# Kernel optimization log

Measured on AMD Instinct MI355X. Metric: run time of the kernel, lower is better.

## Reference

```python
import jax, jax.numpy as jnp
import numpy as np

ZERO_POINT = 128  # asymmetric int8 zero point
LORA_ALPHA = 16.0
LORA_R = 64
LORA_SCALING = LORA_ALPHA / LORA_R


def setup_inputs() -> dict:
    key = jax.random.key(0)
    k_x, k_w, k_s, k_a, k_b, k_bias = jax.random.split(key, 6)
    B, S, D_in, D_out, R = 64, 1, 8192, 8192, LORA_R
    x = jax.random.normal(k_x, (B, S, D_in), dtype=jnp.float32)
    W_q = jax.random.randint(k_w, (D_out, D_in), 0, 256, dtype=jnp.int32)
    scale = jax.random.uniform(k_s, (D_out,), dtype=jnp.float32) * 0.02
    lora_A = jax.random.normal(k_a, (R, D_in), dtype=jnp.float32) * 0.02
    lora_B = jax.random.normal(k_b, (D_out, R), dtype=jnp.float32) * 0.02
    bias = jax.random.normal(k_bias, (D_out,), dtype=jnp.float32)
    return {"x": x, "W_q": W_q, "scale": scale, "lora_A": lora_A,
            "lora_B": lora_B, "bias": bias}


def reference(x, W_q, scale, lora_A, lora_B, bias):
    # Dequantize frozen base weight: per-output-channel asymmetric int8.
    # W_deq[o, i] = (W_q[o, i] - zero_point) * scale[o]
    W_deq = (W_q.astype(jnp.float32) - ZERO_POINT) * scale[:, None]  # [O, I]
    # Base quantized linear: y = x @ W_deq^T + bias
    base = jnp.einsum('bsi,oi->bso', x, W_deq) + bias  # [B, S, O]
    # LoRA low-rank path: (alpha/r) * (x @ A^T) @ B^T  (dropout = 0.0)
    lora_mid = jnp.einsum('bsi,ri->bsr', x, lora_A)        # [B, S, r]
    lora_out = jnp.einsum('bsr,or->bso', lora_mid, lora_B)  # [B, S, O]
    return base + LORA_SCALING * lora_out
```

## Files before the change

### kernel.cpp

```cpp
#include <hip/hip_runtime.h>
#include <stdint.h>

#define B_ 64
#define K_ 8192
#define O_ 8192
#define R_ 64
#define NT 16
#define BK 128
#define NSTEP (K_ / BK)

typedef __attribute__((ext_vector_type(8))) short s16x8;
typedef __attribute__((ext_vector_type(4))) float f32x4;

__device__ __forceinline__ uint32_t rne_pack(float a, float b) {
  uint32_t ua = __float_as_uint(a), ub = __float_as_uint(b);
  ua += 0x7fffu + ((ua >> 16) & 1u);
  ub += 0x7fffu + ((ub >> 16) & 1u);
  return (ua >> 16) | (ub & 0xffff0000u);
}

__device__ __forceinline__ uint32_t wpack(int w0, int w1) {
  float f0 = (float)(w0 - 128);
  float f1 = (float)(w1 - 128);
  return (__float_as_uint(f0) >> 16) | (__float_as_uint(f1) & 0xffff0000u);
}

__global__ __launch_bounds__(256) void k_prep(
    const float* __restrict__ x, const float* __restrict__ lora_A,
    uint16_t* __restrict__ xbg, float* __restrict__ mid) {
  const int t = threadIdx.x;
  const int blk = blockIdx.x;

  {
    const size_t base = (size_t)blk * 2048 + (size_t)t * 8;
    float4 v0 = *(const float4*)(x + base);
    float4 v1 = *(const float4*)(x + base + 4);
    uint4 p;
    p.x = rne_pack(v0.x, v0.y);
    p.y = rne_pack(v0.z, v0.w);
    p.z = rne_pack(v1.x, v1.y);
    p.w = rne_pack(v1.z, v1.w);
    *(uint4*)(xbg + base) = p;
  }

  if (blk >= 64) return;

  __shared__ float xs[64][133];
  __shared__ float as_[64][133];
  const int kr0 = blk * BK;
  const int row = t >> 2, seg = t & 3;
#pragma unroll
  for (int j = 0; j < 8; ++j) {
    const int c = seg * 32 + j * 4;
    float4 vx = *(const float4*)(x + (size_t)row * K_ + kr0 + c);
    float4 va = *(const float4*)(lora_A + (size_t)row * K_ + kr0 + c);
    xs[row][c] = vx.x; xs[row][c + 1] = vx.y; xs[row][c + 2] = vx.z; xs[row][c + 3] = vx.w;
    as_[row][c] = va.x; as_[row][c + 1] = va.y; as_[row][c + 2] = va.z; as_[row][c + 3] = va.w;
  }
  __syncthreads();

  const int bg = t >> 4, rg = t & 15;
  const int b0 = bg * 4, r0 = rg * 4;
  float acc[4][4];
#pragma unroll
  for (int i = 0; i < 4; ++i)
#pragma unroll
    for (int j = 0; j < 4; ++j) acc[i][j] = 0.f;

  for (int k = 0; k < BK; ++k) {
    float xv[4], av[4];
#pragma unroll
    for (int i = 0; i < 4; ++i) xv[i] = xs[b0 + i][k];
#pragma unroll
    for (int j = 0; j < 4; ++j) av[j] = as_[r0 + j][k];
#pragma unroll
    for (int i = 0; i < 4; ++i)
#pragma unroll
      for (int j = 0; j < 4; ++j) acc[i][j] += xv[i] * av[j];
  }

#pragma unroll
  for (int i = 0; i < 4; ++i)
#pragma unroll
    for (int j = 0; j < 4; ++j)
      atomicAdd(&mid[(b0 + i) * R_ + (r0 + j)], acc[i][j]);
}

__global__ __launch_bounds__(256, 2) void k_main(
    const int* __restrict__ Wq, const float* __restrict__ scale,
    const float* __restrict__ lora_B, const float* __restrict__ bias,
    const uint16_t* __restrict__ xbg, const float* __restrict__ mid,
    float* __restrict__ out) {
  __shared__ uint16_t xa[2][64][136];
  __shared__ uint16_t wbs[2][NT][136];
  __shared__ uint16_t midb[64][72];
  __shared__ uint16_t lob[NT][72];

  const int t = threadIdx.x;
  const int o0 = blockIdx.x * NT;
  const int wave = t >> 6;
  const int lane = t & 63;
  const int il = lane & 15;
  const int g = lane >> 4;
  const int m0 = wave * 16;

  {
    const int row = t >> 2;
    const int r0 = (t & 3) * 16;
    const float* mp = mid + row * R_ + r0;
    float4 a0 = *(const float4*)(mp);
    float4 a1 = *(const float4*)(mp + 4);
    float4 a2 = *(const float4*)(mp + 8);
    float4 a3 = *(const float4*)(mp + 12);
    uint4 p0, p1;
    p0.x = rne_pack(a0.x, a0.y); p0.y = rne_pack(a0.z, a0.w);
    p0.z = rne_pack(a1.x, a1.y); p0.w = rne_pack(a1.z, a1.w);
    p1.x = rne_pack(a2.x, a2.y); p1.y = rne_pack(a2.z, a2.w);
    p1.z = rne_pack(a3.x, a3.y); p1.w = rne_pack(a3.z, a3.w);
    *(uint4*)&midb[row][r0] = p0;
    *(uint4*)&midb[row][r0 + 8] = p1;
    if (t < 64) {
      const int row2 = t >> 2;
      const float* lp = lora_B + (size_t)(o0 + row2) * R_ + r0;
      float4 c0 = *(const float4*)(lp);
      float4 c1 = *(const float4*)(lp + 4);
      float4 c2 = *(const float4*)(lp + 8);
      float4 c3 = *(const float4*)(lp + 12);
      uint4 q0, q1;
      q0.x = rne_pack(c0.x, c0.y); q0.y = rne_pack(c0.z, c0.w);
      q0.z = rne_pack(c1.x, c1.y); q0.w = rne_pack(c1.z, c1.w);
      q1.x = rne_pack(c2.x, c2.y); q1.y = rne_pack(c2.z, c2.w);
      q1.z = rne_pack(c3.x, c3.y); q1.w = rne_pack(c3.z, c3.w);
      *(uint4*)&lob[row2][r0] = q0;
      *(uint4*)&lob[row2][r0 + 8] = q1;
    }
  }

  const int xrow = t >> 2, xseg = t & 3;
  const int wrow = t >> 4, wseg = t & 15;
  const uint16_t* xsrc = xbg + (size_t)xrow * K_;
  const int* wsrc = Wq + (size_t)(o0 + wrow) * K_;

  uint4 rx0, rx1, rx2, rx3;
  int4 rw0, rw1;
#define LOADT(TT)                                         \
  do {                                                    \
    const int kt = (TT)*BK;                               \
    rx0 = *(const uint4*)(xsrc + kt + xseg * 32);         \
    rx1 = *(const uint4*)(xsrc + kt + xseg * 32 + 8);     \
    rx2 = *(const uint4*)(xsrc + kt + xseg * 32 + 16);    \
    rx3 = *(const uint4*)(xsrc + kt + xseg * 32 + 24);    \
    rw0 = *(const int4*)(wsrc + kt + wseg * 8);           \
    rw1 = *(const int4*)(wsrc + kt + wseg * 8 + 4);       \
  } while (0)

  LOADT(0);

  const float sc = scale[o0 + il];
  const float bi = bias[o0 + il];

  __syncthreads();

  f32x4 acc2 = {0.f, 0.f, 0.f, 0.f};
#pragma unroll
  for (int kf = 0; kf < 2; ++kf) {
    s16x8 am = *(const s16x8*)&midb[m0 + il][kf * 32 + g * 8];
    s16x8 bl = *(const s16x8*)&lob[il][kf * 32 + g * 8];
    acc2 = __builtin_amdgcn_mfma_f32_16x16x32_bf16(am, bl, acc2, 0, 0, 0);
  }

  f32x4 acc = {0.f, 0.f, 0.f, 0.f};
  int cur = 0;
  for (int tt = 0; tt < NSTEP; ++tt) {
    *(uint4*)&xa[cur][xrow][xseg * 32] = rx0;
    *(uint4*)&xa[cur][xrow][xseg * 32 + 8] = rx1;
    *(uint4*)&xa[cur][xrow][xseg * 32 + 16] = rx2;
    *(uint4*)&xa[cur][xrow][xseg * 32 + 24] = rx3;
    uint4 wv;
    wv.x = wpack(rw0.x, rw0.y);
    wv.y = wpack(rw0.z, rw0.w);
    wv.z = wpack(rw1.x, rw1.y);
    wv.w = wpack(rw1.z, rw1.w);
    *(uint4*)&wbs[cur][wrow][wseg * 8] = wv;
    __syncthreads();
    if (tt + 1 < NSTEP) LOADT(tt + 1);
#pragma unroll
    for (int kf = 0; kf < 4; ++kf) {
      s16x8 af = *(const s16x8*)&xa[cur][m0 + il][kf * 32 + g * 8];
      s16x8 bf = *(const s16x8*)&wbs[cur][il][kf * 32 + g * 8];
      acc = __builtin_amdgcn_mfma_f32_16x16x32_bf16(af, bf, acc, 0, 0, 0);
    }
    cur ^= 1;
  }
#undef LOADT

#pragma unroll
  for (int j = 0; j < 4; ++j) {
    const int b = m0 + g * 4 + j;
    out[(size_t)b * O_ + o0 + il] = sc * acc[j] + bi + 0.25f * acc2[j];
  }
}

extern "C" void kernel_launch(void* const* d_in, const int* in_sizes, int n_in,
                              void* d_out, int out_size, void* d_ws, size_t ws_size,
                              hipStream_t stream) {
  const float* x = (const float*)d_in[0];
  const int* Wq = (const int*)d_in[1];
  const float* scale = (const float*)d_in[2];
  const float* lora_A = (const float*)d_in[3];
  const float* lora_B = (const float*)d_in[4];
  const float* bias = (const float*)d_in[5];
  float* out = (float*)d_out;

  uint16_t* xbg = (uint16_t*)d_ws;
  float* mid = (float*)((char*)d_ws + (size_t)B_ * K_ * 2);

  hipMemsetAsync(mid, 0, B_ * R_ * sizeof(float), stream);
  k_prep<<<256, 256, 0, stream>>>(x, lora_A, xbg, mid);
  k_main<<<O_ / NT, 256, 0, stream>>>(Wq, scale, lora_B, bias, xbg, mid, out);
}
```

Baseline: 92.50 us.

## Prefetch two K-tiles ahead in registers and alias LoRA LDS buffers

The main GEMV loop now keeps two register sets of global loads in flight, so tiles tt+2 and tt+3 load while the current tile runs on MFMA. This deepens the pipeline to hide HBM latency on the int32 weight stream. The global access pattern changes so each lane reads interleaved 16-byte chunks, and the midb/lob LoRA buffers now alias the xa LDS buffer to cut shared memory use. The cost is more live registers (two sets of 6 vector loads) and one extra barrier, which could hurt occupancy at launch_bounds(256,2).

```diff
diff --git a/kernel.cpp b/kernel.cpp
--- a/kernel.cpp
+++ b/kernel.cpp
@@ -93,8 +93,9 @@
     float* __restrict__ out) {
   __shared__ uint16_t xa[2][64][136];
   __shared__ uint16_t wbs[2][NT][136];
-  __shared__ uint16_t midb[64][72];
-  __shared__ uint16_t lob[NT][72];
+
+  uint16_t* midb = &xa[0][0][0];
+  uint16_t* lob = midb + 64 * 72;
 
   const int t = threadIdx.x;
   const int o0 = blockIdx.x * NT;
@@ -117,8 +118,8 @@
     p0.z = rne_pack(a1.x, a1.y); p0.w = rne_pack(a1.z, a1.w);
     p1.x = rne_pack(a2.x, a2.y); p1.y = rne_pack(a2.z, a2.w);
     p1.z = rne_pack(a3.x, a3.y); p1.w = rne_pack(a3.z, a3.w);
-    *(uint4*)&midb[row][r0] = p0;
-    *(uint4*)&midb[row][r0 + 8] = p1;
+    *(uint4*)&midb[row * 72 + r0] = p0;
+    *(uint4*)&midb[row * 72 + r0 + 8] = p1;
     if (t < 64) {
       const int row2 = t >> 2;
       const float* lp = lora_B + (size_t)(o0 + row2) * R_ + r0;
@@ -131,30 +132,57 @@
       q0.z = rne_pack(c1.x, c1.y); q0.w = rne_pack(c1.z, c1.w);
       q1.x = rne_pack(c2.x, c2.y); q1.y = rne_pack(c2.z, c2.w);
       q1.z = rne_pack(c3.x, c3.y); q1.w = rne_pack(c3.z, c3.w);
-      *(uint4*)&lob[row2][r0] = q0;
-      *(uint4*)&lob[row2][r0 + 8] = q1;
+      *(uint4*)&lob[row2 * 72 + r0] = q0;
+      *(uint4*)&lob[row2 * 72 + r0 + 8] = q1;
     }
   }
 
-  const int xrow = t >> 2, xseg = t & 3;
-  const int wrow = t >> 4, wseg = t & 15;
+  const int xrow = t >> 2, xs4 = t & 3;
+  const int wrow = t >> 4, ws16 = t & 15;
   const uint16_t* xsrc = xbg + (size_t)xrow * K_;
   const int* wsrc = Wq + (size_t)(o0 + wrow) * K_;
 
-  uint4 rx0, rx1, rx2, rx3;
-  int4 rw0, rw1;
-#define LOADT(TT)                                         \
-  do {                                                    \
-    const int kt = (TT)*BK;                               \
-    rx0 = *(const uint4*)(xsrc + kt + xseg * 32);         \
-    rx1 = *(const uint4*)(xsrc + kt + xseg * 32 + 8);     \
-    rx2 = *(const uint4*)(xsrc + kt + xseg * 32 + 16);    \
-    rx3 = *(const uint4*)(xsrc + kt + xseg * 32 + 24);    \
-    rw0 = *(const int4*)(wsrc + kt + wseg * 8);           \
-    rw1 = *(const int4*)(wsrc + kt + wseg * 8 + 4);       \
+  uint4 rxa0, rxb0, rxc0, rxd0, rxa1, rxb1, rxc1, rxd1;
+  int4 rwa0, rwb0, rwa1, rwb1;
+
+#define LOADT(P, TT)                                        \
+  do {                                                      \
+    const int kt = (TT)*BK;                                 \
+    rwa##P = *(const int4*)(wsrc + kt + ws16 * 4);          \
+    rwb##P = *(const int4*)(wsrc + kt + 64 + ws16 * 4);     \
+    rxa##P = *(const uint4*)(xsrc + kt + xs4 * 8);          \
+    rxb##P = *(const uint4*)(xsrc + kt + 32 + xs4 * 8);     \
+    rxc##P = *(const uint4*)(xsrc + kt + 64 + xs4 * 8);     \
+    rxd##P = *(const uint4*)(xsrc + kt + 96 + xs4 * 8);     \
   } while (0)
 
-  LOADT(0);
+#define STORE_LDS(P)                                        \
+  do {                                                      \
+    *(uint4*)&xa[P][xrow][xs4 * 8] = rxa##P;                \
+    *(uint4*)&xa[P][xrow][32 + xs4 * 8] = rxb##P;           \
+    *(uint4*)&xa[P][xrow][64 + xs4 * 8] = rxc##P;           \
+    *(uint4*)&xa[P][xrow][96 + xs4 * 8] = rxd##P;           \
+    uint2 wv0, wv1;                                         \
+    wv0.x = wpack(rwa##P.x, rwa##P.y);                      \
+    wv0.y = wpack(rwa##P.z, rwa##P.w);                      \
+    wv1.x = wpack(rwb##P.x, rwb##P.y);                      \
+    wv1.y = wpack(rwb##P.z, rwb##P.w);                      \
+    *(uint2*)&wbs[P][wrow][ws16 * 4] = wv0;                 \
+    *(uint2*)&wbs[P][wrow][64 + ws16 * 4] = wv1;            \
+  } while (0)
+
+#define MFMA_FROM(P)                                                          \
+  do {                                                                        \
+    _Pragma("unroll")                                                         \
+    for (int kf = 0; kf < 4; ++kf) {                                          \
+      s16x8 af = *(const s16x8*)&xa[P][m0 + il][kf * 32 + g * 8];             \
+      s16x8 bf = *(const s16x8*)&wbs[P][il][kf * 32 + g * 8];                 \
+      acc = __builtin_amdgcn_mfma_f32_16x16x32_bf16(af, bf, acc, 0, 0, 0);    \
+    }                                                                         \
+  } while (0)
+
+  LOADT(0, 0);
+  LOADT(1, 1);
 
   const float sc = scale[o0 + il];
   const float bi = bias[o0 + il];
@@ -164,35 +192,27 @@
   f32x4 acc2 = {0.f, 0.f, 0.f, 0.f};
 #pragma unroll
   for (int kf = 0; kf < 2; ++kf) {
-    s16x8 am = *(const s16x8*)&midb[m0 + il][kf * 32 + g * 8];
-    s16x8 bl = *(const s16x8*)&lob[il][kf * 32 + g * 8];
+    s16x8 am = *(const s16x8*)&midb[(m0 + il) * 72 + kf * 32 + g * 8];
+    s16x8 bl = *(const s16x8*)&lob[il * 72 + kf * 32 + g * 8];
     acc2 = __builtin_amdgcn_mfma_f32_16x16x32_bf16(am, bl, acc2, 0, 0, 0);
   }
+  __syncthreads();
 
   f32x4 acc = {0.f, 0.f, 0.f, 0.f};
-  int cur = 0;
-  for (int tt = 0; tt < NSTEP; ++tt) {
-    *(uint4*)&xa[cur][xrow][xseg * 32] = rx0;
-    *(uint4*)&xa[cur][xrow][xseg * 32 + 8] = rx1;
-    *(uint4*)&xa[cur][xrow][xseg * 32 + 16] = rx2;
-    *(uint4*)&xa[cur][xrow][xseg * 32 + 24] = rx3;
-    uint4 wv;
-    wv.x = wpack(rw0.x, rw0.y);
-    wv.y = wpack(rw0.z, rw0.w);
-    wv.z = wpack(rw1.x, rw1.y);
-    wv.w = wpack(rw1.z, rw1.w);
-    *(uint4*)&wbs[cur][wrow][wseg * 8] = wv;
+  for (int tt = 0; tt < NSTEP; tt += 2) {
+    STORE_LDS(0);
     __syncthreads();
-    if (tt + 1 < NSTEP) LOADT(tt + 1);
-#pragma unroll
-    for (int kf = 0; kf < 4; ++kf) {
-      s16x8 af = *(const s16x8*)&xa[cur][m0 + il][kf * 32 + g * 8];
-      s16x8 bf = *(const s16x8*)&wbs[cur][il][kf * 32 + g * 8];
-      acc = __builtin_amdgcn_mfma_f32_16x16x32_bf16(af, bf, acc, 0, 0, 0);
-    }
-    cur ^= 1;
+    if (tt + 2 < NSTEP) LOADT(0, tt + 2);
+    MFMA_FROM(0);
+
+    STORE_LDS(1);
+    __syncthreads();
+    if (tt + 3 < NSTEP) LOADT(1, tt + 3);
+    MFMA_FROM(1);
   }
 #undef LOADT
+#undef STORE_LDS
+#undef MFMA_FROM
 
 #pragma unroll
   for (int j = 0; j < 4; ++j) {
```

New measurement: 88.75 us. 1.04x faster.

## Split-K main GEMM into per-wave register-direct tiles with separate reduction kernel

Applied to the files above, without the earlier changes.

Restructures the main GEMM so each wave owns a 16-output by 64-batch tile over one eighth of K. The wave loads W and x fragments straight from global into registers with two-stage software pipelining and drops the shared-memory staging and block barriers. Partial sums go to a workspace buffer. A new finalize kernel reduces the eight partials and applies scale, bias and the LoRA path. The goal is more parallelism and less LDS/sync overhead, at the cost of about 16 MB of extra partial-sum traffic and one more kernel launch.

```diff
diff --git a/kernel.cpp b/kernel.cpp
--- a/kernel.cpp
+++ b/kernel.cpp
@@ -5,9 +5,10 @@
 #define K_ 8192
 #define O_ 8192
 #define R_ 64
-#define NT 16
-#define BK 128
-#define NSTEP (K_ / BK)
+#define KS 8
+#define KSL (K_ / KS)
+#define BK 64
+#define NS (KSL / BK)
 
 typedef __attribute__((ext_vector_type(8))) short s16x8;
 typedef __attribute__((ext_vector_type(4))) float f32x4;
@@ -23,6 +24,17 @@
   float f0 = (float)(w0 - 128);
   float f1 = (float)(w1 - 128);
   return (__float_as_uint(f0) >> 16) | (__float_as_uint(f1) & 0xffff0000u);
+}
+
+__device__ __forceinline__ s16x8 bfrag_from(int4 a, int4 b) {
+  union { uint32_t u[4]; s16x8 v; } r;
+  r.u[0] = wpack(a.x, a.y); r.u[1] = wpack(a.z, a.w);
+  r.u[2] = wpack(b.x, b.y); r.u[3] = wpack(b.z, b.w);
+  return r.v;
+}
+
+__device__ __forceinline__ s16x8 afrag(uint4 x) {
+  union { uint4 u; s16x8 v; } r; r.u = x; return r.v;
 }
 
 __global__ __launch_bounds__(256) void k_prep(
@@ -47,7 +59,7 @@
 
   __shared__ float xs[64][133];
   __shared__ float as_[64][133];
-  const int kr0 = blk * BK;
+  const int kr0 = blk * 128;
   const int row = t >> 2, seg = t & 3;
 #pragma unroll
   for (int j = 0; j < 8; ++j) {
@@ -67,7 +79,7 @@
 #pragma unroll
     for (int j = 0; j < 4; ++j) acc[i][j] = 0.f;
 
-  for (int k = 0; k < BK; ++k) {
+  for (int k = 0; k < 128; ++k) {
     float xv[4], av[4];
 #pragma unroll
     for (int i = 0; i < 4; ++i) xv[i] = xs[b0 + i][k];
@@ -87,17 +99,95 @@
 }
 
 __global__ __launch_bounds__(256, 2) void k_main(
-    const int* __restrict__ Wq, const float* __restrict__ scale,
+    const int* __restrict__ Wq, const uint16_t* __restrict__ xbg,
+    float* __restrict__ part) {
+  const int t = threadIdx.x;
+  const int w = blockIdx.x * 4 + (t >> 6);
+  const int lane = t & 63;
+  const int il = lane & 15;
+  const int g = lane >> 4;
+  const int ks = w >> 9;
+  const int oc = w & 511;
+  const int o0 = oc * 16;
+  const int k0 = ks * KSL;
+
+  const int* wp = Wq + (size_t)(o0 + il) * K_ + k0 + g * 8;
+  const uint16_t* xp0 = xbg + (size_t)(il) * K_ + k0 + g * 8;
+  const uint16_t* xp1 = xbg + (size_t)(16 + il) * K_ + k0 + g * 8;
+  const uint16_t* xp2 = xbg + (size_t)(32 + il) * K_ + k0 + g * 8;
+  const uint16_t* xp3 = xbg + (size_t)(48 + il) * K_ + k0 + g * 8;
+
+  f32x4 ac0 = {0.f,0.f,0.f,0.f}, ac1 = {0.f,0.f,0.f,0.f};
+  f32x4 ac2 = {0.f,0.f,0.f,0.f}, ac3 = {0.f,0.f,0.f,0.f};
+
+  int4 rw00a, rw00b, rw01a, rw01b, rw10a, rw10b, rw11a, rw11b;
+  uint4 rx000, rx001, rx010, rx011, rx020, rx021, rx030, rx031;
+  uint4 rx100, rx101, rx110, rx111, rx120, rx121, rx130, rx131;
+
+#define LOADS(P, S)                                                   \
+  do {                                                                \
+    const int c0 = (S) * BK, c1 = (S) * BK + 32;                      \
+    rw##P##0a = *(const int4*)(wp + c0);                              \
+    rw##P##0b = *(const int4*)(wp + c0 + 4);                          \
+    rw##P##1a = *(const int4*)(wp + c1);                              \
+    rw##P##1b = *(const int4*)(wp + c1 + 4);                          \
+    rx##P##00 = *(const uint4*)(xp0 + c0);                            \
+    rx##P##01 = *(const uint4*)(xp0 + c1);                            \
+    rx##P##10 = *(const uint4*)(xp1 + c0);                            \
+    rx##P##11 = *(const uint4*)(xp1 + c1);                            \
+    rx##P##20 = *(const uint4*)(xp2 + c0);                            \
+    rx##P##21 = *(const uint4*)(xp2 + c1);                            \
+    rx##P##30 = *(const uint4*)(xp3 + c0);                            \
+    rx##P##31 = *(const uint4*)(xp3 + c1);                            \
+  } while (0)
+
+#define MFMAS(P)                                                               \
+  do {                                                                         \
+    s16x8 bf0 = bfrag_from(rw##P##0a, rw##P##0b);                              \
+    ac0 = __builtin_amdgcn_mfma_f32_16x16x32_bf16(afrag(rx##P##00), bf0, ac0, 0, 0, 0); \
+    ac1 = __builtin_amdgcn_mfma_f32_16x16x32_bf16(afrag(rx##P##10), bf0, ac1, 0, 0, 0); \
+    ac2 = __builtin_amdgcn_mfma_f32_16x16x32_bf16(afrag(rx##P##20), bf0, ac2, 0, 0, 0); \
+    ac3 = __builtin_amdgcn_mfma_f32_16x16x32_bf16(afrag(rx##P##30), bf0, ac3, 0, 0, 0); \
+    s16x8 bf1 = bfrag_from(rw##P##1a, rw##P##1b);                              \
+    ac0 = __builtin_amdgcn_mfma_f32_16x16x32_bf16(afrag(rx##P##01), bf1, ac0, 0, 0, 0); \
+    ac1 = __builtin_amdgcn_mfma_f32_16x16x32_bf16(afrag(rx##P##11), bf1, ac1, 0, 0, 0); \
+    ac2 = __builtin_amdgcn_mfma_f32_16x16x32_bf16(afrag(rx##P##21), bf1, ac2, 0, 0, 0); \
+    ac3 = __builtin_amdgcn_mfma_f32_16x16x32_bf16(afrag(rx##P##31), bf1, ac3, 0, 0, 0); \
+  } while (0)
+
+  LOADS(0, 0);
+  LOADS(1, 1);
+
+#pragma unroll
+  for (int s = 0; s < NS; s += 2) {
+    MFMAS(0);
+    if (s + 2 < NS) LOADS(0, s + 2);
+    MFMAS(1);
+    if (s + 3 < NS) LOADS(1, s + 3);
+  }
+#undef LOADS
+#undef MFMAS
+
+  float* pp = part + (size_t)ks * (B_ * O_) + o0 + il;
+#pragma unroll
+  for (int j = 0; j < 4; ++j) {
+    const int r = g * 4 + j;
+    pp[(size_t)(r) * O_]      = ac0[j];
+    pp[(size_t)(16 + r) * O_] = ac1[j];
+    pp[(size_t)(32 + r) * O_] = ac2[j];
+    pp[(size_t)(48 + r) * O_] = ac3[j];
+  }
+}
+
+__global__ __launch_bounds__(256) void k_fin(
+    const float* __restrict__ part, const float* __restrict__ scale,
     const float* __restrict__ lora_B, const float* __restrict__ bias,
-    const uint16_t* __restrict__ xbg, const float* __restrict__ mid,
-    float* __restrict__ out) {
-  __shared__ uint16_t xa[2][64][136];
-  __shared__ uint16_t wbs[2][NT][136];
+    const float* __restrict__ mid, float* __restrict__ out) {
   __shared__ uint16_t midb[64][72];
-  __shared__ uint16_t lob[NT][72];
+  __shared__ uint16_t lob[16][72];
 
   const int t = threadIdx.x;
-  const int o0 = blockIdx.x * NT;
+  const int o0 = blockIdx.x * 16;
   const int wave = t >> 6;
   const int lane = t & 63;
   const int il = lane & 15;
@@ -135,30 +225,6 @@
       *(uint4*)&lob[row2][r0 + 8] = q1;
     }
   }
-
-  const int xrow = t >> 2, xseg = t & 3;
-  const int wrow = t >> 4, wseg = t & 15;
-  const uint16_t* xsrc = xbg + (size_t)xrow * K_;
-  const int* wsrc = Wq + (size_t)(o0 + wrow) * K_;
-
-  uint4 rx0, rx1, rx2, rx3;
-  int4 rw0, rw1;
-#define LOADT(TT)                                         \
-  do {                                                    \
-    const int kt = (TT)*BK;                               \
-    rx0 = *(const uint4*)(xsrc + kt + xseg * 32);         \
-    rx1 = *(const uint4*)(xsrc + kt + xseg * 32 + 8);     \
-    rx2 = *(const uint4*)(xsrc + kt + xseg * 32 + 16);    \
-    rx3 = *(const uint4*)(xsrc + kt + xseg * 32 + 24);    \
-    rw0 = *(const int4*)(wsrc + kt + wseg * 8);           \
-    rw1 = *(const int4*)(wsrc + kt + wseg * 8 + 4);       \
-  } while (0)
-
-  LOADT(0);
-
-  const float sc = scale[o0 + il];
-  const float bi = bias[o0 + il];
-
   __syncthreads();
 
   f32x4 acc2 = {0.f, 0.f, 0.f, 0.f};
@@ -169,35 +235,17 @@
     acc2 = __builtin_amdgcn_mfma_f32_16x16x32_bf16(am, bl, acc2, 0, 0, 0);
   }
 
-  f32x4 acc = {0.f, 0.f, 0.f, 0.f};
-  int cur = 0;
-  for (int tt = 0; tt < NSTEP; ++tt) {
-    *(uint4*)&xa[cur][xrow][xseg * 32] = rx0;
-    *(uint4*)&xa[cur][xrow][xseg * 32 + 8] = rx1;
-    *(uint4*)&xa[cur][xrow][xseg * 32 + 16] = rx2;
-    *(uint4*)&xa[cur][xrow][xseg * 32 + 24] = rx3;
-    uint4 wv;
-    wv.x = wpack(rw0.x, rw0.y);
-    wv.y = wpack(rw0.z, rw0.w);
-    wv.z = wpack(rw1.x, rw1.y);
-    wv.w = wpack(rw1.z, rw1.w);
-    *(uint4*)&wbs[cur][wrow][wseg * 8] = wv;
-    __syncthreads();
-    if (tt + 1 < NSTEP) LOADT(tt + 1);
-#pragma unroll
-    for (int kf = 0; kf < 4; ++kf) {
-      s16x8 af = *(const s16x8*)&xa[cur][m0 + il][kf * 32 + g * 8];
-      s16x8 bf = *(const s16x8*)&wbs[cur][il][kf * 32 + g * 8];
-      acc = __builtin_amdgcn_mfma_f32_16x16x32_bf16(af, bf, acc, 0, 0, 0);
-    }
-    cur ^= 1;
-  }
-#undef LOADT
+  const float sc = scale[o0 + il];
+  const float bi = bias[o0 + il];
 
 #pragma unroll
   for (int j = 0; j < 4; ++j) {
     const int b = m0 + g * 4 + j;
-    out[(size_t)b * O_ + o0 + il] = sc * acc[j] + bi + 0.25f * acc2[j];
+    const size_t idx = (size_t)b * O_ + o0 + il;
+    float s = 0.f;
+#pragma unroll
+    for (int k = 0; k < KS; ++k) s += part[(size_t)k * (B_ * O_) + idx];
+    out[idx] = sc * s + bi + 0.25f * acc2[j];
   }
 }
 
@@ -213,9 +261,11 @@
   float* out = (float*)d_out;
 
   uint16_t* xbg = (uint16_t*)d_ws;
-  float* mid = (float*)((char*)d_ws + (size_t)B_ * K_ * 2);
+  float* mid = (float*)((char*)d_ws + (2u << 20));
+  float* part = (float*)((char*)d_ws + (4u << 20));
 
   hipMemsetAsync(mid, 0, B_ * R_ * sizeof(float), stream);
   k_prep<<<256, 256, 0, stream>>>(x, lora_A, xbg, mid);
-  k_main<<<O_ / NT, 256, 0, stream>>>(Wq, scale, lora_B, bias, xbg, mid, out);
-}
+  k_main<<<(KS * (O_ / 16)) / 4, 256, 0, stream>>>(Wq, xbg, part);
+  k_fin<<<O_ / 16, 256, 0, stream>>>(part, scale, lora_B, bias, mid, out);
+}
```

New measurement: 130.2 us. +40.7%, slower.

## Split-K main GEMM, load x fragments directly to registers, add finalize kernel

Applied to the files above, without the earlier changes.

Splits the K dimension in two so the grid doubles (1024 blocks) and raises the occupancy hint to 4 blocks per SM. The x operand is no longer staged through LDS; each lane loads its MFMA A fragment straight from global into registers, with a deeper software pipeline (4 weight stages and 2 x stages in flight). The LoRA, scale and bias epilogue moves to a new finalize kernel that sums the two partials. This adds an extra launch and 4 MB of partial writes and reads, and the 4-blocks-per-SM bound may limit registers.

```diff
diff --git a/kernel.cpp b/kernel.cpp
--- a/kernel.cpp
+++ b/kernel.cpp
@@ -6,8 +6,10 @@
 #define O_ 8192
 #define R_ 64
 #define NT 16
+#define KSP 2
+#define KHALF (K_ / KSP)
 #define BK 128
-#define NSTEP (K_ / BK)
+#define NS2 (KHALF / BK)
 
 typedef __attribute__((ext_vector_type(8))) short s16x8;
 typedef __attribute__((ext_vector_type(4))) float f32x4;
@@ -23,6 +25,10 @@
   float f0 = (float)(w0 - 128);
   float f1 = (float)(w1 - 128);
   return (__float_as_uint(f0) >> 16) | (__float_as_uint(f1) & 0xffff0000u);
+}
+
+__device__ __forceinline__ s16x8 afrag(uint4 x) {
+  union { uint4 u; s16x8 v; } r; r.u = x; return r.v;
 }
 
 __global__ __launch_bounds__(256) void k_prep(
@@ -47,7 +53,7 @@
 
   __shared__ float xs[64][133];
   __shared__ float as_[64][133];
-  const int kr0 = blk * BK;
+  const int kr0 = blk * 128;
   const int row = t >> 2, seg = t & 3;
 #pragma unroll
   for (int j = 0; j < 8; ++j) {
@@ -67,7 +73,7 @@
 #pragma unroll
     for (int j = 0; j < 4; ++j) acc[i][j] = 0.f;
 
-  for (int k = 0; k < BK; ++k) {
+  for (int k = 0; k < 128; ++k) {
     float xv[4], av[4];
 #pragma unroll
     for (int i = 0; i < 4; ++i) xv[i] = xs[b0 + i][k];
@@ -86,18 +92,92 @@
       atomicAdd(&mid[(b0 + i) * R_ + (r0 + j)], acc[i][j]);
 }
 
-__global__ __launch_bounds__(256, 2) void k_main(
-    const int* __restrict__ Wq, const float* __restrict__ scale,
+__global__ __launch_bounds__(256, 4) void k_main(
+    const int* __restrict__ Wq, const uint16_t* __restrict__ xbg,
+    float* __restrict__ part) {
+  __shared__ uint16_t wbs[2][NT][132];
+
+  const int t = threadIdx.x;
+  const int oc = blockIdx.x >> 1;
+  const int ks = blockIdx.x & 1;
+  const int o0 = oc * NT;
+  const int k0 = ks * KHALF;
+
+  const int wave = t >> 6, lane = t & 63, il = lane & 15, g = lane >> 4;
+  const int m0 = wave * 16;
+  const int wrow = t >> 4, wseg = t & 15;
+
+  const int* wsrc = Wq + (size_t)(o0 + wrow) * K_ + k0 + wseg * 8;
+  const uint16_t* xq = xbg + (size_t)(m0 + il) * K_ + k0 + g * 8;
+
+  int4 rwa0, rwb0, rwa1, rwb1, rwa2, rwb2, rwa3, rwb3;
+  uint4 ax00, ax01, ax02, ax03, ax10, ax11, ax12, ax13;
+
+#define LOADW(P, S)                                  \
+  do {                                               \
+    rwa##P = *(const int4*)(wsrc + (S)*BK);          \
+    rwb##P = *(const int4*)(wsrc + (S)*BK + 4);      \
+  } while (0)
+#define LOADX(Q, S)                                  \
+  do {                                               \
+    ax##Q##0 = *(const uint4*)(xq + (S)*BK);         \
+    ax##Q##1 = *(const uint4*)(xq + (S)*BK + 32);    \
+    ax##Q##2 = *(const uint4*)(xq + (S)*BK + 64);    \
+    ax##Q##3 = *(const uint4*)(xq + (S)*BK + 96);    \
+  } while (0)
+
+  f32x4 acc = {0.f, 0.f, 0.f, 0.f};
+
+  LOADW(0, 0); LOADW(1, 1); LOADW(2, 2); LOADW(3, 3);
+  LOADX(0, 0); LOADX(1, 1);
+
+#define PHASE(P, Q)                                                            \
+  do {                                                                         \
+    const int S = s + P;                                                       \
+    uint4 wv;                                                                  \
+    wv.x = wpack(rwa##P.x, rwa##P.y); wv.y = wpack(rwa##P.z, rwa##P.w);        \
+    wv.z = wpack(rwb##P.x, rwb##P.y); wv.w = wpack(rwb##P.z, rwb##P.w);        \
+    *(uint4*)&wbs[S & 1][wrow][wseg * 8] = wv;                                 \
+    if (S + 4 < NS2) LOADW(P, S + 4);                                          \
+    asm volatile("s_waitcnt lgkmcnt(0)" ::: "memory");                         \
+    __builtin_amdgcn_s_barrier();                                              \
+    __builtin_amdgcn_sched_barrier(0);                                         \
+    s16x8 bf0 = *(const s16x8*)&wbs[S & 1][il][0 * 32 + g * 8];                \
+    acc = __builtin_amdgcn_mfma_f32_16x16x32_bf16(afrag(ax##Q##0), bf0, acc, 0, 0, 0); \
+    s16x8 bf1 = *(const s16x8*)&wbs[S & 1][il][1 * 32 + g * 8];                \
+    acc = __builtin_amdgcn_mfma_f32_16x16x32_bf16(afrag(ax##Q##1), bf1, acc, 0, 0, 0); \
+    s16x8 bf2 = *(const s16x8*)&wbs[S & 1][il][2 * 32 + g * 8];                \
+    acc = __builtin_amdgcn_mfma_f32_16x16x32_bf16(afrag(ax##Q##2), bf2, acc, 0, 0, 0); \
+    s16x8 bf3 = *(const s16x8*)&wbs[S & 1][il][3 * 32 + g * 8];                \
+    acc = __builtin_amdgcn_mfma_f32_16x16x32_bf16(afrag(ax##Q##3), bf3, acc, 0, 0, 0); \
+    if (S + 2 < NS2) LOADX(Q, S + 2);                                          \
+  } while (0)
+
+  for (int s = 0; s < NS2; s += 4) {
+    PHASE(0, 0);
+    PHASE(1, 1);
+    PHASE(2, 0);
+    PHASE(3, 1);
+  }
+#undef LOADW
+#undef LOADX
+#undef PHASE
+
+  float* pp = part + (size_t)ks * (B_ * O_) + o0 + il;
+#pragma unroll
+  for (int j = 0; j < 4; ++j)
+    pp[(size_t)(m0 + g * 4 + j) * O_] = acc[j];
+}
+
+__global__ __launch_bounds__(256) void k_fin(
+    const float* __restrict__ part, const float* __restrict__ scale,
     const float* __restrict__ lora_B, const float* __restrict__ bias,
-    const uint16_t* __restrict__ xbg, const float* __restrict__ mid,
-    float* __restrict__ out) {
-  __shared__ uint16_t xa[2][64][136];
-  __shared__ uint16_t wbs[2][NT][136];
+    const float* __restrict__ mid, float* __restrict__ out) {
   __shared__ uint16_t midb[64][72];
-  __shared__ uint16_t lob[NT][72];
+  __shared__ uint16_t lob[16][72];
 
   const int t = threadIdx.x;
-  const int o0 = blockIdx.x * NT;
+  const int o0 = blockIdx.x * 16;
   const int wave = t >> 6;
   const int lane = t & 63;
   const int il = lane & 15;
@@ -135,30 +215,6 @@
       *(uint4*)&lob[row2][r0 + 8] = q1;
     }
   }
-
-  const int xrow = t >> 2, xseg = t & 3;
-  const int wrow = t >> 4, wseg = t & 15;
-  const uint16_t* xsrc = xbg + (size_t)xrow * K_;
-  const int* wsrc = Wq + (size_t)(o0 + wrow) * K_;
-
-  uint4 rx0, rx1, rx2, rx3;
-  int4 rw0, rw1;
-#define LOADT(TT)                                         \
-  do {                                                    \
-    const int kt = (TT)*BK;                               \
-    rx0 = *(const uint4*)(xsrc + kt + xseg * 32);         \
-    rx1 = *(const uint4*)(xsrc + kt + xseg * 32 + 8);     \
-    rx2 = *(const uint4*)(xsrc + kt + xseg * 32 + 16);    \
-    rx3 = *(const uint4*)(xsrc + kt + xseg * 32 + 24);    \
-    rw0 = *(const int4*)(wsrc + kt + wseg * 8);           \
-    rw1 = *(const int4*)(wsrc + kt + wseg * 8 + 4);       \
-  } while (0)
-
-  LOADT(0);
-
-  const float sc = scale[o0 + il];
-  const float bi = bias[o0 + il];
-
   __syncthreads();
 
   f32x4 acc2 = {0.f, 0.f, 0.f, 0.f};
@@ -169,35 +225,15 @@
     acc2 = __builtin_amdgcn_mfma_f32_16x16x32_bf16(am, bl, acc2, 0, 0, 0);
   }
 
-  f32x4 acc = {0.f, 0.f, 0.f, 0.f};
-  int cur = 0;
-  for (int tt = 0; tt < NSTEP; ++tt) {
-    *(uint4*)&xa[cur][xrow][xseg * 32] = rx0;
-    *(uint4*)&xa[cur][xrow][xseg * 32 + 8] = rx1;
-    *(uint4*)&xa[cur][xrow][xseg * 32 + 16] = rx2;
-    *(uint4*)&xa[cur][xrow][xseg * 32 + 24] = rx3;
-    uint4 wv;
-    wv.x = wpack(rw0.x, rw0.y);
-    wv.y = wpack(rw0.z, rw0.w);
-    wv.z = wpack(rw1.x, rw1.y);
-    wv.w = wpack(rw1.z, rw1.w);
-    *(uint4*)&wbs[cur][wrow][wseg * 8] = wv;
-    __syncthreads();
-    if (tt + 1 < NSTEP) LOADT(tt + 1);
-#pragma unroll
-    for (int kf = 0; kf < 4; ++kf) {
-      s16x8 af = *(const s16x8*)&xa[cur][m0 + il][kf * 32 + g * 8];
-      s16x8 bf = *(const s16x8*)&wbs[cur][il][kf * 32 + g * 8];
-      acc = __builtin_amdgcn_mfma_f32_16x16x32_bf16(af, bf, acc, 0, 0, 0);
-    }
-    cur ^= 1;
-  }
-#undef LOADT
+  const float sc = scale[o0 + il];
+  const float bi = bias[o0 + il];
 
 #pragma unroll
   for (int j = 0; j < 4; ++j) {
     const int b = m0 + g * 4 + j;
-    out[(size_t)b * O_ + o0 + il] = sc * acc[j] + bi + 0.25f * acc2[j];
+    const size_t idx = (size_t)b * O_ + o0 + il;
+    float s = part[idx] + part[(size_t)(B_ * O_) + idx];
+    out[idx] = sc * s + bi + 0.25f * acc2[j];
   }
 }
 
@@ -213,9 +249,11 @@
   float* out = (float*)d_out;
 
   uint16_t* xbg = (uint16_t*)d_ws;
-  float* mid = (float*)((char*)d_ws + (size_t)B_ * K_ * 2);
+  float* mid = (float*)((char*)d_ws + (2u << 20));
+  float* part = (float*)((char*)d_ws + (4u << 20));
 
   hipMemsetAsync(mid, 0, B_ * R_ * sizeof(float), stream);
   k_prep<<<256, 256, 0, stream>>>(x, lora_A, xbg, mid);
-  k_main<<<O_ / NT, 256, 0, stream>>>(Wq, scale, lora_B, bias, xbg, mid, out);
-}
+  k_main<<<KSP * (O_ / NT), 256, 0, stream>>>(Wq, xbg, part);
+  k_fin<<<O_ / 16, 256, 0, stream>>>(part, scale, lora_B, bias, mid, out);
+}
```

After: 103.4 us. +11.7%, slower.
